# Kernel optimization log

Measured on AMD Instinct MI355X. Metric: run time of the kernel, lower is better.

## Reference

```python
import jax, jax.numpy as jnp
import numpy as np

# Model hyper-parameters (from CMRET __init__ defaults)
N_A, F, H, K, NK, L = 4096, 128, 4, 15, 50, 6
CUTOFF, TEMP, BOX, N_Z = 5.0, 2.0, 40.0, 100
DH = F // H  # per-head dim


def setup_inputs() -> dict:
    key = jax.random.key(0)
    ks = jax.random.split(key, 12)
    Z = jax.random.randint(ks[0], (1, N_A), 0, N_Z)
    R = jax.random.uniform(ks[1], (1, N_A, 3), dtype=jnp.float32) * BOX
    batch = jnp.ones((1, N_A, 1), jnp.float32)
    g = lambda k, shp, s: jax.random.normal(k, shp, jnp.float32) * s
    emb = g(ks[2], (N_Z, F), 1.0)
    Wq = g(ks[3], (L, F, F), F ** -0.5)
    Wk = g(ks[4], (L, F, F), F ** -0.5)
    Wv = g(ks[5], (L, F, 3 * F), F ** -0.5)
    We_k = g(ks[6], (L, NK, F), NK ** -0.5)
    be_k = jnp.zeros((L, F), jnp.float32)
    We_v = g(ks[7], (L, NK, 3 * F), NK ** -0.5)
    be_v = jnp.zeros((L, 3 * F), jnp.float32)
    ln_g = jnp.ones((F,), jnp.float32)
    ln_b = jnp.zeros((F,), jnp.float32)
    Wo1 = g(ks[8], (F, F), F ** -0.5)
    Wo2 = g(ks[9], (F, 1), F ** -0.5)
    return dict(Z=Z, R=R, batch=batch, emb=emb, Wq=Wq, Wk=Wk, Wv=Wv,
                We_k=We_k, be_k=be_k, We_v=We_v, be_v=be_v,
                ln_g=ln_g, ln_b=ln_b, Wo1=Wo1, Wo2=Wo2)


def reference(Z, R, batch, emb, Wq, Wk, Wv, We_k, be_k, We_v, be_v, ln_g, ln_b, Wo1, Wo2):
    n_a = Z.shape[1]
    r = R[0]                                  # (n_a, 3)
    b = batch[..., 0]                         # (1, n_a)
    bm = (b.T @ b) == 0                       # (n_a, n_a) cross-molecule mask
    # --- Distance: k-nearest-neighbour selection (gather-based) ---
    sq = jnp.sum(r * r, -1)
    d2 = sq[:, None] + sq[None, :] - 2.0 * (r @ r.T)
    d2 = jnp.where(bm | jnp.eye(n_a, dtype=bool), 1e9, jnp.maximum(d2, 0.0))
    _, idxs = jax.lax.top_k(-d2, K)           # (n_a, K) neighbour indices
    vec = r[idxs] - r[:, None, :]             # (n_a, K, 3)
    d = jnp.sqrt(jnp.sum(vec * vec, -1) + 1e-12)
    vec_norm = vec / d[..., None]
    # --- Gaussian RBF * cosine cutoff edge features ---
    mu = jnp.linspace(0.0, CUTOFF, NK, dtype=jnp.float32)
    delta = CUTOFF / NK
    cut = 0.5 * (jnp.cos(jnp.pi * d / CUTOFF) + 1.0) * (d <= CUTOFF)
    e = jnp.exp(-((d[..., None] - mu) ** 2) / (2.0 * delta * delta)) * cut[..., None]
    # --- embedding and channel init ---
    s = emb[Z[0]]                             # (n_a, F) scalar channel
    o = jnp.zeros_like(s)                     # residual accumulator
    v = jnp.zeros((n_a, 3, F), s.dtype)       # vector channel
    scale = jnp.asarray(1.0 / np.sqrt(DH * TEMP), jnp.float32)
    # --- attention interaction stack ---
    for l in range(L):
        q = (s @ Wq[l]).reshape(n_a, H, DH)
        kk = s @ Wk[l]
        val = s @ Wv[l]                       # (n_a, 3F)
        ek = jax.nn.silu(e @ We_k[l] + be_k[l])   # (n_a, K, F) edge key filter
        ev = jax.nn.silu(e @ We_v[l] + be_v[l])   # (n_a, K, 3F) edge value filter
        kh = (kk[idxs] * ek).reshape(n_a, K, H, DH)
        logits = jnp.einsum('nhd,nkhd->nkh', q, kh) * scale
        attn = jax.nn.softmax(logits, axis=1) * cut[..., None]
        wf = jnp.repeat(attn, DH, axis=-1)        # (n_a, K, F) per-channel weights
        m1, m2, m3 = jnp.split(val[idxs] * ev, 3, axis=-1)
        ds = jnp.sum(wf * m1, axis=1)             # scalar message (n_a, F)
        dv = jnp.sum((wf * m2)[:, :, None, :] * vec_norm[..., None]
                     + (wf * m3)[:, :, None, :] * v[idxs], axis=1)
        s = s + ds
        o = o + ds
        v = v + dv
    # --- final LayerNorm + readout ---
    mean = o.mean(-1, keepdims=True)
    var = o.var(-1, keepdims=True)
    o = (o - mean) / jnp.sqrt(var + 1e-5) * ln_g + ln_b
    h = jax.nn.silu(o @ Wo1) @ Wo2            # (n_a, 1) per-atom contribution
    return jnp.sum(h * batch[0], axis=0, keepdims=True)  # (1, 1) energy
```

## Files before the change

### kernel.cpp

```cpp
#include <hip/hip_runtime.h>
#include <math.h>

#define NATOMS 4096
#define FDIM   128
#define NHEAD  4
#define DHEAD  32
#define KNBR   15
#define NKER   50
#define NLAYER 6
#define QKVW   640

typedef __attribute__((ext_vector_type(8))) short short8;
typedef __attribute__((ext_vector_type(4))) float f32x4;

__device__ __forceinline__ float silu_f(float x) { return x / (1.0f + __expf(-x)); }

__device__ __forceinline__ unsigned long long shfl_xor_u64(unsigned long long v, int m) {
    unsigned lo = (unsigned)v, hi = (unsigned)(v >> 32);
    lo = (unsigned)__shfl_xor((int)lo, m);
    hi = (unsigned)__shfl_xor((int)hi, m);
    return ((unsigned long long)hi << 32) | lo;
}
__device__ __forceinline__ unsigned long long min_u64(unsigned long long a, unsigned long long b) {
    return a < b ? a : b;
}
__device__ __forceinline__ int spread3(int v) {
    return (v & 1) | ((v & 2) << 2) | ((v & 4) << 4) | ((v & 8) << 6);
}

__global__ __launch_bounds__(1024) void morton_kernel(
    const float* __restrict__ R, int* __restrict__ perm, int* __restrict__ rank)
{
    __shared__ int hist[4096];
    __shared__ int tscan[1024];
    const int t = threadIdx.x;
    int codes[4];
    #pragma unroll
    for (int u = 0; u < 4; ++u) hist[t*4 + u] = 0;
    __syncthreads();
    #pragma unroll
    for (int u = 0; u < 4; ++u) {
        int i = t + u*1024;
        float x = R[i*3+0], y = R[i*3+1], z = R[i*3+2];
        int cx = min(15, max(0, (int)(x * (16.0f/40.0f))));
        int cy = min(15, max(0, (int)(y * (16.0f/40.0f))));
        int cz = min(15, max(0, (int)(z * (16.0f/40.0f))));
        int code = spread3(cx) | (spread3(cy) << 1) | (spread3(cz) << 2);
        codes[u] = code;
        atomicAdd(&hist[code], 1);
    }
    __syncthreads();
    int loc[4], s0 = 0;
    #pragma unroll
    for (int u = 0; u < 4; ++u) { loc[u] = hist[t*4 + u]; s0 += loc[u]; }
    tscan[t] = s0;
    __syncthreads();
    for (int off = 1; off < 1024; off <<= 1) {
        int v = tscan[t];
        int a = (t >= off) ? tscan[t - off] : 0;
        __syncthreads();
        tscan[t] = v + a;
        __syncthreads();
    }
    int run = tscan[t] - s0;
    #pragma unroll
    for (int u = 0; u < 4; ++u) { hist[t*4 + u] = run; run += loc[u]; }
    __syncthreads();
    #pragma unroll
    for (int u = 0; u < 4; ++u) {
        int i = t + u*1024;
        int r = atomicAdd(&hist[codes[u]], 1);
        perm[r] = i;
        rank[i] = r;
    }
}

__global__ __launch_bounds__(256) void knn_kernel(
    const float* __restrict__ R, const float* __restrict__ batch,
    const int* __restrict__ perm, const int* __restrict__ rank,
    int* __restrict__ idxs, float* __restrict__ cutw,
    float* __restrict__ vecn, float* __restrict__ ebuf)
{
    __shared__ float d2s[NATOMS];
    __shared__ unsigned long long wred[2][4];
    __shared__ int sel[KNBR];
    const int r = blockIdx.x, t = threadIdx.x;
    const int i = perm[r];
    const int wave = t >> 6, lane = t & 63;
    const float xi = R[i*3+0], yi = R[i*3+1], zi = R[i*3+2];
    const float bi = batch[i];
    const float sqi = xi*xi + yi*yi + zi*zi;
    for (int j = t; j < NATOMS; j += 256) {
        float xj = R[j*3+0], yj = R[j*3+1], zj = R[j*3+2];
        float sqj = xj*xj + yj*yj + zj*zj;
        float d2 = sqi + sqj - 2.0f*(xi*xj + yi*yj + zi*zj);
        if (bi*batch[j] == 0.0f || j == i) d2 = 1e9f;
        else d2 = fmaxf(d2, 0.0f);
        d2s[j] = d2;
    }
    __syncthreads();

    unsigned long long cand = ~0ull;
    #pragma unroll
    for (int it = 0; it < 16; ++it) {
        int j = t + it*256;
        unsigned long long p = ((unsigned long long)__float_as_uint(d2s[j]) << 32) | (unsigned)j;
        cand = min_u64(cand, p);
    }
    for (int k = 0; k < KNBR; ++k) {
        unsigned long long w = cand;
        #pragma unroll
        for (int off = 1; off < 64; off <<= 1)
            w = min_u64(w, shfl_xor_u64(w, off));
        if (lane == 0) wred[k & 1][wave] = w;
        __syncthreads();
        unsigned long long f = min_u64(min_u64(wred[k&1][0], wred[k&1][1]),
                                       min_u64(wred[k&1][2], wred[k&1][3]));
        int sj = (int)(unsigned)f;
        if (t == 0) sel[k] = sj;
        if ((sj & 255) == t) {
            d2s[sj] = 1e9f;
            cand = ~0ull;
            #pragma unroll
            for (int it = 0; it < 16; ++it) {
                int j = t + it*256;
                unsigned long long p = ((unsigned long long)__float_as_uint(d2s[j]) << 32) | (unsigned)j;
                cand = min_u64(cand, p);
            }
        }
    }
    __syncthreads();

    if (t < KNBR) {
        int j = sel[t];
        idxs[r*KNBR + t] = rank[j];
        float vx = R[j*3+0]-xi, vy = R[j*3+1]-yi, vz = R[j*3+2]-zi;
        float d = sqrtf(vx*vx + vy*vy + vz*vz + 1e-12f);
        float inv = 1.0f/d;
        vecn[(r*KNBR+t)*3+0] = vx*inv;
        vecn[(r*KNBR+t)*3+1] = vy*inv;
        vecn[(r*KNBR+t)*3+2] = vz*inv;
        const float PI = 3.14159265358979323846f;
        float cutv = (d <= 5.0f) ? 0.5f*(cosf(PI*d*0.2f) + 1.0f) : 0.0f;
        cutw[r*KNBR + t] = cutv;
        for (int jj = 0; jj < NKER; ++jj) {
            float mu = 5.0f * (float)jj / 49.0f;
            float dd = d - mu;
            ebuf[(r*KNBR+t)*NKER + jj] = __expf(-dd*dd*50.0f) * cutv;
        }
    }
}

__global__ __launch_bounds__(256) void init_kernel(
    const int* __restrict__ Z, const float* __restrict__ emb,
    const int* __restrict__ perm,
    float* __restrict__ s, float* __restrict__ o, float* __restrict__ v0)
{
    int stride = gridDim.x * blockDim.x;
    for (int idx = blockIdx.x*blockDim.x + threadIdx.x; idx < NATOMS*3*FDIM; idx += stride) {
        v0[idx] = 0.0f;
        if (idx < NATOMS*FDIM) {
            int a = idx >> 7, c = idx & 127;
            s[idx] = emb[Z[perm[a]]*FDIM + c];
            o[idx] = 0.0f;
        }
    }
}

__global__ __launch_bounds__(64) void wprep_kernel(
    const float* __restrict__ WeK, const float* __restrict__ WeV,
    unsigned short* __restrict__ Wswz)
{
    const int blk = blockIdx.x;
    const int lane = threadIdx.x;
    const int ks = blk & 1;
    const int T  = (blk >> 1) & 31;
    const int l  = blk >> 6;
    const int quad = lane >> 4, x = lane & 15;
    unsigned short* dst = Wswz + (size_t)blk*1024 + lane*8;
    for (int j = 0; j < 8; ++j) {
        int k = ks*32 + quad*8 + j;
        float w = 0.0f;
        if (k < NKER)
            w = (T < 8) ? WeK[l*NKER*FDIM + k*FDIM + T*16 + x]
                        : WeV[(size_t)l*NKER*3*FDIM + k*3*FDIM + (T-8)*16 + x];
        unsigned b = __float_as_uint(w);
        dst[j] = (unsigned short)(b >> 16);
        float r = w - __uint_as_float(b & 0xFFFF0000u);
        dst[512 + j] = (unsigned short)(__float_as_uint(r) >> 16);
    }
}

__global__ __launch_bounds__(64) void qprep_kernel(
    const float* __restrict__ Wq, const float* __restrict__ Wk,
    const float* __restrict__ Wv, unsigned short* __restrict__ Qswz)
{
    const int blk = blockIdx.x;
    const int lane = threadIdx.x;
    const int ks = blk & 3;
    const int ct = (blk >> 2) % 40;
    const int l  = blk / 160;
    const int quad = lane >> 4, lx = lane & 15;
    const int col = ct*16 + lx;
    unsigned short* dst = Qswz + (size_t)blk*1024 + lane*8;
    for (int j = 0; j < 8; ++j) {
        int k = ks*32 + quad*8 + j;
        float w;
        if (col < 128)      w = Wq[l*16384 + k*128 + col];
        else if (col < 256) w = Wk[l*16384 + k*128 + (col-128)];
        else                w = Wv[(size_t)l*49152 + k*384 + (col-256)];
        unsigned b = __float_as_uint(w);
        dst[j] = (unsigned short)(b >> 16);
        float r = w - __uint_as_float(b & 0xFFFF0000u);
        dst[512 + j] = (unsigned short)(__float_as_uint(r) >> 16);
    }
}

__global__ __launch_bounds__(128) void proj_kernel(
    const float* __restrict__ S, const unsigned short* __restrict__ Qswz,
    float* __restrict__ QKV, int l)
{
    const int rt = blockIdx.x;
    const int t = threadIdx.x, wave = t >> 6, lane = t & 63;
    const int quad = lane >> 4, lx = lane & 15;
    const int cg = blockIdx.y*2 + wave;

    short8 ah[4], al[4];
    const float* srow = S + (size_t)(rt*16 + lx)*FDIM;
    #pragma unroll
    for (int ks = 0; ks < 4; ++ks) {
        float v[8];
        *(f32x4*)&v[0] = *(const f32x4*)(srow + ks*32 + quad*8);
        *(f32x4*)&v[4] = *(const f32x4*)(srow + ks*32 + quad*8 + 4);
        #pragma unroll
        for (int j = 0; j < 8; ++j) {
            unsigned b = __float_as_uint(v[j]);
            ah[ks][j] = (short)(b >> 16);
            float r = v[j] - __uint_as_float(b & 0xFFFF0000u);
            al[ks][j] = (short)(__float_as_uint(r) >> 16);
        }
    }
    for (int ci = 0; ci < 10; ++ci) {
        const int ct = cg*10 + ci;
        const unsigned short* wp = Qswz + (size_t)((l*40 + ct)*4)*1024 + lane*8;
        f32x4 acc = {0.0f, 0.0f, 0.0f, 0.0f};
        #pragma unroll
        for (int ks = 0; ks < 4; ++ks) {
            short8 bh = *(const short8*)(wp + ks*1024);
            short8 bl = *(const short8*)(wp + ks*1024 + 512);
            acc = __builtin_amdgcn_mfma_f32_16x16x32_bf16(ah[ks], bh, acc, 0, 0, 0);
            acc = __builtin_amdgcn_mfma_f32_16x16x32_bf16(ah[ks], bl, acc, 0, 0, 0);
            acc = __builtin_amdgcn_mfma_f32_16x16x32_bf16(al[ks], bh, acc, 0, 0, 0);
        }
        const int col = ct*16 + lx;
        #pragma unroll
        for (int r = 0; r < 4; ++r)
            QKV[(size_t)(rt*16 + quad*4 + r)*QKVW + col] = acc[r];
    }
}

__global__ __launch_bounds__(512) void attn_kernel(
    const float* __restrict__ QKV, const int* __restrict__ idxs,
    const float* __restrict__ cutw, const float* __restrict__ vecn,
    const float* __restrict__ ebuf, const unsigned short* __restrict__ Wswz,
    const float* __restrict__ beK, const float* __restrict__ beV,
    float* __restrict__ s, float* __restrict__ o,
    const float* __restrict__ vin, float* __restrict__ vout, int l)
{
    __shared__ __align__(16) float es[16][68];
    __shared__ __align__(16) float fbuf[KNBR][516];
    __shared__ int   nidx[KNBR];
    __shared__ float cutv[KNBR];
    __shared__ float vnc[KNBR][3];
    __shared__ float attns[KNBR][NHEAD];
    __shared__ float dvbuf[3][FDIM];

    const int i = blockIdx.x, t = threadIdx.x;
    const int wave = t >> 6, lane = t & 63;
    const int quad = lane >> 4, lx = lane & 15;

    if (t < KNBR) {
        nidx[t] = idxs[i*KNBR + t];
        cutv[t] = cutw[i*KNBR + t];
        vnc[t][0] = vecn[(i*KNBR+t)*3+0];
        vnc[t][1] = vecn[(i*KNBR+t)*3+1];
        vnc[t][2] = vecn[(i*KNBR+t)*3+2];
    }
    for (int x = t; x < 16*64; x += 512) {
        int row = x >> 6, col = x & 63;
        es[row][col] = (row < KNBR && col < NKER)
                       ? ebuf[(size_t)i*KNBR*NKER + row*NKER + col] : 0.0f;
    }
    __syncthreads();

    for (int x = t; x < KNBR*128; x += 512) {
        int k = x >> 7, c4 = x & 127;
        *(f32x4*)&fbuf[k][c4*4] =
            *(const f32x4*)(QKV + (size_t)nidx[k]*QKVW + FDIM + c4*4);
    }

    short8 eh[2], el[2];
    #pragma unroll
    for (int ks = 0; ks < 2; ++ks) {
        float v[8];
        *(f32x4*)&v[0] = *(const f32x4*)&es[lx][ks*32 + quad*8];
        *(f32x4*)&v[4] = *(const f32x4*)&es[lx][ks*32 + quad*8 + 4];
        #pragma unroll
        for (int j = 0; j < 8; ++j) {
            unsigned b = __float_as_uint(v[j]);
            eh[ks][j] = (short)(b >> 16);
            float r = v[j] - __uint_as_float(b & 0xFFFF0000u);
            el[ks][j] = (short)(__float_as_uint(r) >> 16);
        }
    }
    __syncthreads();

    #pragma unroll
    for (int tt = 0; tt < 4; ++tt) {
        const int T = wave*4 + tt;
        const int col = T*16 + lx;
        f32x4 acc = {0.0f, 0.0f, 0.0f, 0.0f};
        #pragma unroll
        for (int ks = 0; ks < 2; ++ks) {
            const unsigned short* wp = Wswz + ((size_t)((l*32+T)*2+ks))*1024 + lane*8;
            short8 bh = *(const short8*)wp;
            short8 bl = *(const short8*)(wp + 512);
            acc = __builtin_amdgcn_mfma_f32_16x16x32_bf16(eh[ks], bh, acc, 0, 0, 0);
            acc = __builtin_amdgcn_mfma_f32_16x16x32_bf16(eh[ks], bl, acc, 0, 0, 0);
            acc = __builtin_amdgcn_mfma_f32_16x16x32_bf16(el[ks], bh, acc, 0, 0, 0);
        }
        const float b = (col < FDIM) ? beK[l*FDIM + col]
                                     : beV[(size_t)l*3*FDIM + (col - FDIM)];
        #pragma unroll
        for (int r = 0; r < 4; ++r) {
            int k = quad*4 + r;
            if (k < KNBR) {
                float f = silu_f(acc[r] + b);
                fbuf[k][col] = f * fbuf[k][col];
            }
        }
    }
    __syncthreads();

    if (t < FDIM) {
        const int c = t, h = c >> 5;
        const float q = QKV[(size_t)i*QKVW + c];
        float lg[KNBR];
        #pragma unroll
        for (int k = 0; k < KNBR; ++k) {
            float p = q * fbuf[k][c];
            p += __shfl_xor(p, 1);
            p += __shfl_xor(p, 2);
            p += __shfl_xor(p, 4);
            p += __shfl_xor(p, 8);
            p += __shfl_xor(p, 16);
            lg[k] = p * 0.125f;
        }
        float m = -1e30f;
        #pragma unroll
        for (int k = 0; k < KNBR; ++k) m = fmaxf(m, lg[k]);
        float ssum = 0.0f;
        #pragma unroll
        for (int k = 0; k < KNBR; ++k) { lg[k] = __expf(lg[k]-m); ssum += lg[k]; }
        float inv = 1.0f/ssum;
        if ((c & 31) == 0) {
            #pragma unroll
            for (int k = 0; k < KNBR; ++k) attns[k][h] = lg[k]*inv*cutv[k];
        }
    }
    float mval[KNBR];
    int cv = 0, h2 = 0;
    if (t >= FDIM) {
        cv = t - FDIM; h2 = (cv & 127) >> 5;
        #pragma unroll
        for (int k = 0; k < KNBR; ++k) mval[k] = fbuf[k][FDIM + cv];
    }
    __syncthreads();

    if (t >= FDIM) {
        if (cv < FDIM) {
            float ds = 0.0f;
            #pragma unroll
            for (int k = 0; k < KNBR; ++k) ds += attns[k][h2]*mval[k];
            s[i*FDIM + cv] += ds;
            o[i*FDIM + cv] += ds;
        } else if (cv < 2*FDIM) {
            const int cc = cv - FDIM;
            float d0 = 0.0f, d1 = 0.0f, d2 = 0.0f;
            #pragma unroll
            for (int k = 0; k < KNBR; ++k) {
                float w = attns[k][h2]*mval[k];
                d0 += w*vnc[k][0]; d1 += w*vnc[k][1]; d2 += w*vnc[k][2];
            }
            dvbuf[0][cc] = d0; dvbuf[1][cc] = d1; dvbuf[2][cc] = d2;
        }
    }
    float d3[3] = {0.0f, 0.0f, 0.0f};
    if (t >= FDIM && cv >= 2*FDIM) {
        const int cc = cv - 2*FDIM;
        #pragma unroll
        for (int k = 0; k < KNBR; ++k) {
            float w = attns[k][h2]*mval[k];
            const float* vb = vin + (size_t)nidx[k]*3*FDIM + cc;
            d3[0] += w*vb[0*FDIM]; d3[1] += w*vb[1*FDIM]; d3[2] += w*vb[2*FDIM];
        }
    }
    __syncthreads();
    if (t >= FDIM && cv >= 2*FDIM) {
        const int cc = cv - 2*FDIM;
        #pragma unroll
        for (int x = 0; x < 3; ++x) {
            size_t off = (size_t)i*3*FDIM + x*FDIM + cc;
            vout[off] = vin[off] + dvbuf[x][cc] + d3[x];
        }
    }
}

__global__ __launch_bounds__(128) void final_kernel(
    const float* __restrict__ o, const float* __restrict__ lng, const float* __restrict__ lnb,
    const float* __restrict__ Wo1, const float* __restrict__ Wo2,
    const float* __restrict__ batch, const int* __restrict__ perm,
    float* __restrict__ hout)
{
    __shared__ float red[128];
    __shared__ float on[128];
    const int i = blockIdx.x, t = threadIdx.x;
    float x = o[i*FDIM + t];
    red[t] = x; __syncthreads();
    for (int off = 64; off > 0; off >>= 1) { if (t < off) red[t] += red[t+off]; __syncthreads(); }
    float mean = red[0] * (1.0f/128.0f);
    __syncthreads();
    float xm = x - mean;
    red[t] = xm*xm; __syncthreads();
    for (int off = 64; off > 0; off >>= 1) { if (t < off) red[t] += red[t+off]; __syncthreads(); }
    float var = red[0] * (1.0f/128.0f);
    __syncthreads();
    on[t] = xm * rsqrtf(var + 1e-5f) * lng[t] + lnb[t];
    __syncthreads();
    float acc = 0.0f;
    #pragma unroll 8
    for (int j = 0; j < 128; ++j) acc += on[j] * Wo1[j*128 + t];
    float h = silu_f(acc) * Wo2[t];
    red[t] = h; __syncthreads();
    for (int off = 64; off > 0; off >>= 1) { if (t < off) red[t] += red[t+off]; __syncthreads(); }
    if (t == 0) hout[i] = red[0] * batch[perm[i]];
}

__global__ __launch_bounds__(1024) void reduce_kernel(
    const float* __restrict__ hout, float* __restrict__ out)
{
    __shared__ float red[1024];
    const int t = threadIdx.x;
    float a = hout[t] + hout[t+1024] + hout[t+2048] + hout[t+3072];
    red[t] = a; __syncthreads();
    for (int off = 512; off > 0; off >>= 1) {
        if (t < off) red[t] += red[t+off];
        __syncthreads();
    }
    if (t == 0) out[0] = red[0];
}

extern "C" void kernel_launch(void* const* d_in, const int* in_sizes, int n_in,
                              void* d_out, int out_size, void* d_ws, size_t ws_size,
                              hipStream_t stream)
{
    const int*   Z     = (const int*)  d_in[0];
    const float* R     = (const float*)d_in[1];
    const float* batch = (const float*)d_in[2];
    const float* emb   = (const float*)d_in[3];
    const float* Wq    = (const float*)d_in[4];
    const float* Wk    = (const float*)d_in[5];
    const float* Wv    = (const float*)d_in[6];
    const float* WeK   = (const float*)d_in[7];
    const float* beK   = (const float*)d_in[8];
    const float* WeV   = (const float*)d_in[9];
    const float* beV   = (const float*)d_in[10];
    const float* lng   = (const float*)d_in[11];
    const float* lnb   = (const float*)d_in[12];
    const float* Wo1   = (const float*)d_in[13];
    const float* Wo2   = (const float*)d_in[14];
    float* out = (float*)d_out;

    float* fws = (float*)d_ws;
    float* s    = fws; fws += NATOMS*FDIM;
    float* o    = fws; fws += NATOMS*FDIM;
    float* v0   = fws; fws += NATOMS*3*FDIM;
    float* v1   = fws; fws += NATOMS*3*FDIM;
    float* qkv  = fws; fws += NATOMS*QKVW;
    float* cutw = fws; fws += NATOMS*KNBR;
    float* vecn = fws; fws += NATOMS*KNBR*3;
    float* ebuf = fws; fws += NATOMS*KNBR*NKER;
    float* hout = fws; fws += NATOMS;
    int*   idxs = (int*)fws; fws += NATOMS*KNBR;
    int*   perm = (int*)fws; fws += NATOMS;
    int*   rank = (int*)fws; fws += NATOMS;
    unsigned short* Wswz = (unsigned short*)fws;
    fws += (NLAYER*32*2*1024) / 2;
    unsigned short* Qswz = (unsigned short*)fws;

    morton_kernel<<<1, 1024, 0, stream>>>(R, perm, rank);
    wprep_kernel<<<NLAYER*32*2, 64, 0, stream>>>(WeK, WeV, Wswz);
    qprep_kernel<<<NLAYER*40*4, 64, 0, stream>>>(Wq, Wk, Wv, Qswz);
    knn_kernel<<<NATOMS, 256, 0, stream>>>(R, batch, perm, rank, idxs, cutw, vecn, ebuf);
    init_kernel<<<1024, 256, 0, stream>>>(Z, emb, perm, s, o, v0);
    for (int l = 0; l < NLAYER; ++l) {
        proj_kernel<<<dim3(256, 2), 128, 0, stream>>>(s, Qswz, qkv, l);
        float* vin  = (l & 1) ? v1 : v0;
        float* vout = (l & 1) ? v0 : v1;
        attn_kernel<<<NATOMS, 512, 0, stream>>>(qkv, idxs, cutw, vecn, ebuf, Wswz,
                                                beK, beV, s, o, vin, vout, l);
    }
    final_kernel<<<NATOMS, 128, 0, stream>>>(o, lng, lnb, Wo1, Wo2, batch, perm, hout);
    reduce_kernel<<<1, 1024, 0, stream>>>(hout, out);
}
```

Baseline: 571.3 us.

## Precompute bf16-split edge operands in knn and rebalance attention message work

The knn kernel now converts the RBF edge features into the swizzled hi/lo bf16 MFMA operand layout once and stores them, so each attention layer loads ready-made short8 fragments. This removes the per-layer edge staging in LDS and the bf16 split. The gathered neighbour K/V rows are now read straight from global memory at the filter multiply instead of being staged into LDS first. The message phase is rebalanced so all 512 threads do work: the v-gather over neighbours is split across two thread groups and combined through an extra LDS buffer, which costs more scattered global loads in exchange for better thread utilisation and fewer barriers.

Result: faster. 520.7 us (-8.9%).

```diff
diff --git a/kernel.cpp b/kernel.cpp
--- a/kernel.cpp
+++ b/kernel.cpp
@@ -79,9 +79,10 @@
     const float* __restrict__ R, const float* __restrict__ batch,
     const int* __restrict__ perm, const int* __restrict__ rank,
     int* __restrict__ idxs, float* __restrict__ cutw,
-    float* __restrict__ vecn, float* __restrict__ ebuf)
+    float* __restrict__ vecn, unsigned short* __restrict__ eA)
 {
     __shared__ float d2s[NATOMS];
+    __shared__ float e_lds[16][64];
     __shared__ unsigned long long wred[2][4];
     __shared__ int sel[KNBR];
     const int r = blockIdx.x, t = threadIdx.x;
@@ -90,6 +91,7 @@
     const float xi = R[i*3+0], yi = R[i*3+1], zi = R[i*3+2];
     const float bi = batch[i];
     const float sqi = xi*xi + yi*yi + zi*zi;
+    for (int x = t; x < 16*64; x += 256) ((float*)e_lds)[x] = 0.0f;
     for (int j = t; j < NATOMS; j += 256) {
         float xj = R[j*3+0], yj = R[j*3+1], zj = R[j*3+2];
         float sqj = xj*xj + yj*yj + zj*zj;
@@ -146,8 +148,27 @@
         for (int jj = 0; jj < NKER; ++jj) {
             float mu = 5.0f * (float)jj / 49.0f;
             float dd = d - mu;
-            ebuf[(r*KNBR+t)*NKER + jj] = __expf(-dd*dd*50.0f) * cutv;
-        }
+            e_lds[t][jj] = __expf(-dd*dd*50.0f) * cutv;
+        }
+    }
+    __syncthreads();
+
+    {
+        const int l2 = t & 63, grp = t >> 6;
+        const int ks = grp >> 1, part = grp & 1;
+        const int lx = l2 & 15, quad = l2 >> 4;
+        short8 vv;
+        #pragma unroll
+        for (int j = 0; j < 8; ++j) {
+            float v = e_lds[lx][ks*32 + quad*8 + j];
+            unsigned b = __float_as_uint(v);
+            if (part == 0) vv[j] = (short)(b >> 16);
+            else {
+                float rr = v - __uint_as_float(b & 0xFFFF0000u);
+                vv[j] = (short)(__float_as_uint(rr) >> 16);
+            }
+        }
+        *(short8*)(eA + (size_t)r*2048 + grp*512 + l2*8) = vv;
     }
 }
 
@@ -262,18 +283,18 @@
 __global__ __launch_bounds__(512) void attn_kernel(
     const float* __restrict__ QKV, const int* __restrict__ idxs,
     const float* __restrict__ cutw, const float* __restrict__ vecn,
-    const float* __restrict__ ebuf, const unsigned short* __restrict__ Wswz,
+    const unsigned short* __restrict__ eA, const unsigned short* __restrict__ Wswz,
     const float* __restrict__ beK, const float* __restrict__ beV,
     float* __restrict__ s, float* __restrict__ o,
     const float* __restrict__ vin, float* __restrict__ vout, int l)
 {
-    __shared__ __align__(16) float es[16][68];
     __shared__ __align__(16) float fbuf[KNBR][516];
     __shared__ int   nidx[KNBR];
     __shared__ float cutv[KNBR];
     __shared__ float vnc[KNBR][3];
     __shared__ float attns[KNBR][NHEAD];
     __shared__ float dvbuf[3][FDIM];
+    __shared__ float dvbuf2[3][FDIM];
 
     const int i = blockIdx.x, t = threadIdx.x;
     const int wave = t >> 6, lane = t & 63;
@@ -286,33 +307,12 @@
         vnc[t][1] = vecn[(i*KNBR+t)*3+1];
         vnc[t][2] = vecn[(i*KNBR+t)*3+2];
     }
-    for (int x = t; x < 16*64; x += 512) {
-        int row = x >> 6, col = x & 63;
-        es[row][col] = (row < KNBR && col < NKER)
-                       ? ebuf[(size_t)i*KNBR*NKER + row*NKER + col] : 0.0f;
-    }
-    __syncthreads();
-
-    for (int x = t; x < KNBR*128; x += 512) {
-        int k = x >> 7, c4 = x & 127;
-        *(f32x4*)&fbuf[k][c4*4] =
-            *(const f32x4*)(QKV + (size_t)nidx[k]*QKVW + FDIM + c4*4);
-    }
-
+    const unsigned short* ea = eA + (size_t)i*2048 + lane*8;
     short8 eh[2], el[2];
-    #pragma unroll
-    for (int ks = 0; ks < 2; ++ks) {
-        float v[8];
-        *(f32x4*)&v[0] = *(const f32x4*)&es[lx][ks*32 + quad*8];
-        *(f32x4*)&v[4] = *(const f32x4*)&es[lx][ks*32 + quad*8 + 4];
-        #pragma unroll
-        for (int j = 0; j < 8; ++j) {
-            unsigned b = __float_as_uint(v[j]);
-            eh[ks][j] = (short)(b >> 16);
-            float r = v[j] - __uint_as_float(b & 0xFFFF0000u);
-            el[ks][j] = (short)(__float_as_uint(r) >> 16);
-        }
-    }
+    eh[0] = *(const short8*)(ea + 0*512);
+    el[0] = *(const short8*)(ea + 1*512);
+    eh[1] = *(const short8*)(ea + 2*512);
+    el[1] = *(const short8*)(ea + 3*512);
     __syncthreads();
 
     #pragma unroll
@@ -331,17 +331,20 @@
         }
         const float b = (col < FDIM) ? beK[l*FDIM + col]
                                      : beV[(size_t)l*3*FDIM + (col - FDIM)];
+        const int goff = (col < FDIM) ? (FDIM + col) : (2*FDIM + (col - FDIM));
         #pragma unroll
         for (int r = 0; r < 4; ++r) {
             int k = quad*4 + r;
             if (k < KNBR) {
                 float f = silu_f(acc[r] + b);
-                fbuf[k][col] = f * fbuf[k][col];
+                float g = QKV[(size_t)nidx[k]*QKVW + goff];
+                fbuf[k][col] = f * g;
             }
         }
     }
     __syncthreads();
 
+    float pre[KNBR];
     if (t < FDIM) {
         const int c = t, h = c >> 5;
         const float q = QKV[(size_t)i*QKVW + c];
@@ -367,51 +370,60 @@
             #pragma unroll
             for (int k = 0; k < KNBR; ++k) attns[k][h] = lg[k]*inv*cutv[k];
         }
-    }
-    float mval[KNBR];
-    int cv = 0, h2 = 0;
-    if (t >= FDIM) {
-        cv = t - FDIM; h2 = (cv & 127) >> 5;
-        #pragma unroll
-        for (int k = 0; k < KNBR; ++k) mval[k] = fbuf[k][FDIM + cv];
-    }
-    __syncthreads();
-
-    if (t >= FDIM) {
-        if (cv < FDIM) {
-            float ds = 0.0f;
-            #pragma unroll
-            for (int k = 0; k < KNBR; ++k) ds += attns[k][h2]*mval[k];
-            s[i*FDIM + cv] += ds;
-            o[i*FDIM + cv] += ds;
-        } else if (cv < 2*FDIM) {
-            const int cc = cv - FDIM;
-            float d0 = 0.0f, d1 = 0.0f, d2 = 0.0f;
-            #pragma unroll
-            for (int k = 0; k < KNBR; ++k) {
-                float w = attns[k][h2]*mval[k];
-                d0 += w*vnc[k][0]; d1 += w*vnc[k][1]; d2 += w*vnc[k][2];
-            }
-            dvbuf[0][cc] = d0; dvbuf[1][cc] = d1; dvbuf[2][cc] = d2;
-        }
-    }
+    } else if (t < 2*FDIM) {
+        const int cc = t - FDIM;
+        #pragma unroll
+        for (int k = 0; k < KNBR; ++k) pre[k] = fbuf[k][2*FDIM + cc];
+    } else {
+        const int cc = (t < 3*FDIM) ? (t - 2*FDIM) : (t - 3*FDIM);
+        #pragma unroll
+        for (int k = 0; k < KNBR; ++k) pre[k] = fbuf[k][3*FDIM + cc];
+    }
+    __syncthreads();
+
     float d3[3] = {0.0f, 0.0f, 0.0f};
-    if (t >= FDIM && cv >= 2*FDIM) {
-        const int cc = cv - 2*FDIM;
+    if (t < FDIM) {
+        const int c = t, h = c >> 5;
+        float ds = 0.0f;
+        #pragma unroll
+        for (int k = 0; k < KNBR; ++k) ds += attns[k][h]*fbuf[k][FDIM + c];
+        s[i*FDIM + c] += ds;
+        o[i*FDIM + c] += ds;
+    } else if (t < 2*FDIM) {
+        const int cc = t - FDIM, h = cc >> 5;
+        float d0 = 0.0f, d1 = 0.0f, d2 = 0.0f;
         #pragma unroll
         for (int k = 0; k < KNBR; ++k) {
-            float w = attns[k][h2]*mval[k];
+            float w = attns[k][h]*pre[k];
+            d0 += w*vnc[k][0]; d1 += w*vnc[k][1]; d2 += w*vnc[k][2];
+        }
+        dvbuf[0][cc] = d0; dvbuf[1][cc] = d1; dvbuf[2][cc] = d2;
+    } else if (t < 3*FDIM) {
+        const int cc = t - 2*FDIM, h = cc >> 5;
+        #pragma unroll
+        for (int k = 0; k < 8; ++k) {
+            float w = attns[k][h]*pre[k];
             const float* vb = vin + (size_t)nidx[k]*3*FDIM + cc;
             d3[0] += w*vb[0*FDIM]; d3[1] += w*vb[1*FDIM]; d3[2] += w*vb[2*FDIM];
         }
-    }
-    __syncthreads();
-    if (t >= FDIM && cv >= 2*FDIM) {
-        const int cc = cv - 2*FDIM;
+    } else {
+        const int cc = t - 3*FDIM, h = cc >> 5;
+        float e0 = 0.0f, e1 = 0.0f, e2 = 0.0f;
+        #pragma unroll
+        for (int k = 8; k < KNBR; ++k) {
+            float w = attns[k][h]*pre[k];
+            const float* vb = vin + (size_t)nidx[k]*3*FDIM + cc;
+            e0 += w*vb[0*FDIM]; e1 += w*vb[1*FDIM]; e2 += w*vb[2*FDIM];
+        }
+        dvbuf2[0][cc] = e0; dvbuf2[1][cc] = e1; dvbuf2[2][cc] = e2;
+    }
+    __syncthreads();
+    if (t >= 2*FDIM && t < 3*FDIM) {
+        const int cc = t - 2*FDIM;
         #pragma unroll
         for (int x = 0; x < 3; ++x) {
             size_t off = (size_t)i*3*FDIM + x*FDIM + cc;
-            vout[off] = vin[off] + dvbuf[x][cc] + d3[x];
+            vout[off] = vin[off] + dvbuf[x][cc] + dvbuf2[x][cc] + d3[x];
         }
     }
 }
@@ -489,11 +501,12 @@
     float* qkv  = fws; fws += NATOMS*QKVW;
     float* cutw = fws; fws += NATOMS*KNBR;
     float* vecn = fws; fws += NATOMS*KNBR*3;
-    float* ebuf = fws; fws += NATOMS*KNBR*NKER;
     float* hout = fws; fws += NATOMS;
     int*   idxs = (int*)fws; fws += NATOMS*KNBR;
     int*   perm = (int*)fws; fws += NATOMS;
     int*   rank = (int*)fws; fws += NATOMS;
+    unsigned short* eA   = (unsigned short*)fws;
+    fws += (NATOMS*2048) / 2;
     unsigned short* Wswz = (unsigned short*)fws;
     fws += (NLAYER*32*2*1024) / 2;
     unsigned short* Qswz = (unsigned short*)fws;
@@ -501,13 +514,13 @@
     morton_kernel<<<1, 1024, 0, stream>>>(R, perm, rank);
     wprep_kernel<<<NLAYER*32*2, 64, 0, stream>>>(WeK, WeV, Wswz);
     qprep_kernel<<<NLAYER*40*4, 64, 0, stream>>>(Wq, Wk, Wv, Qswz);
-    knn_kernel<<<NATOMS, 256, 0, stream>>>(R, batch, perm, rank, idxs, cutw, vecn, ebuf);
+    knn_kernel<<<NATOMS, 256, 0, stream>>>(R, batch, perm, rank, idxs, cutw, vecn, eA);
     init_kernel<<<1024, 256, 0, stream>>>(Z, emb, perm, s, o, v0);
     for (int l = 0; l < NLAYER; ++l) {
         proj_kernel<<<dim3(256, 2), 128, 0, stream>>>(s, Qswz, qkv, l);
         float* vin  = (l & 1) ? v1 : v0;
         float* vout = (l & 1) ? v0 : v1;
-        attn_kernel<<<NATOMS, 512, 0, stream>>>(qkv, idxs, cutw, vecn, ebuf, Wswz,
+        attn_kernel<<<NATOMS, 512, 0, stream>>>(qkv, idxs, cutw, vecn, eA, Wswz,
                                                 beK, beV, s, o, vin, vout, l);
     }
     final_kernel<<<NATOMS, 128, 0, stream>>>(o, lng, lnb, Wo1, Wo2, batch, perm, hout);
```
